# Kernel optimization log

Hardware: AMD Instinct MI355X
Metric: run time of the kernel (lower is better)

The kernel has to match this reference:

```python
import jax, jax.numpy as jnp
import numpy as np

B, S, V, E, H, A, L = 64, 256, 32000, 512, 512, 512, 2
EPS = 1e-5


def _ln(x, g, b):
    m = jnp.mean(x, axis=-1, keepdims=True)
    v = jnp.mean((x - m) ** 2, axis=-1, keepdims=True)
    return (x - m) * jax.lax.rsqrt(v + EPS) * g + b


def _lstm_cell(x, h, c, W_ih, W_hh, b_ih, b_hh):
    # torch gate order: i, f, g, o
    gates = x @ W_ih.T + b_ih + h @ W_hh.T + b_hh  # [B, 4H]
    i, f, g, o = jnp.split(gates, 4, axis=-1)
    i, f, o = jax.nn.sigmoid(i), jax.nn.sigmoid(f), jax.nn.sigmoid(o)
    g = jnp.tanh(g)
    c_new = f * c + i * g
    h_new = o * jnp.tanh(c_new)
    return h_new, c_new


def setup_inputs() -> dict:
    key = jax.random.key(0)
    ks = jax.random.split(key, 24)
    d = {}
    d['input_token'] = jax.random.randint(ks[0], (B, 1), 0, V)
    d['h0'] = jax.random.normal(ks[1], (L, B, H), jnp.float32)
    d['c0'] = jax.random.normal(ks[2], (L, B, H), jnp.float32)
    d['encoder_outputs'] = jax.random.normal(ks[3], (B, S, 2 * H), jnp.float32)
    d['encoder_mask'] = jnp.ones((B, S), jnp.int32)
    sc = lambda fi, fo: float(np.sqrt(6.0 / (fi + fo)))
    d['emb'] = jax.random.normal(ks[4], (V, E), jnp.float32) * 0.1
    d['ln_emb_g'] = jnp.ones((E,), jnp.float32)
    d['ln_emb_b'] = jnp.zeros((E,), jnp.float32)
    d['W_enc'] = jax.random.uniform(ks[5], (A, 2 * H), jnp.float32, -sc(2 * H, A), sc(2 * H, A))
    d['b_enc'] = jnp.zeros((A,), jnp.float32)
    d['W_dec'] = jax.random.uniform(ks[6], (A, H), jnp.float32, -sc(H, A), sc(H, A))
    d['b_dec'] = jnp.zeros((A,), jnp.float32)
    d['v_att'] = jax.random.uniform(ks[7], (1, A), jnp.float32, -sc(A, 1), sc(A, 1))
    d['ln_att_g'] = jnp.ones((A,), jnp.float32)
    d['ln_att_b'] = jnp.zeros((A,), jnp.float32)
    in0, in1 = E + 2 * H, H
    d['W_ih0'] = jax.random.uniform(ks[8], (4 * H, in0), jnp.float32, -sc(in0, 4 * H), sc(in0, 4 * H))
    d['W_hh0'] = jax.random.normal(ks[9], (4 * H, H), jnp.float32) * 0.05
    d['b_ih0'] = jnp.zeros((4 * H,), jnp.float32).at[H:2 * H].set(1.0)
    d['b_hh0'] = jnp.zeros((4 * H,), jnp.float32)
    d['W_ih1'] = jax.random.uniform(ks[10], (4 * H, in1), jnp.float32, -sc(in1, 4 * H), sc(in1, 4 * H))
    d['W_hh1'] = jax.random.normal(ks[11], (4 * H, H), jnp.float32) * 0.05
    d['b_ih1'] = jnp.zeros((4 * H,), jnp.float32).at[H:2 * H].set(1.0)
    d['b_hh1'] = jnp.zeros((4 * H,), jnp.float32)
    d['ln_lstm_g'] = jnp.ones((H,), jnp.float32)
    d['ln_lstm_b'] = jnp.zeros((H,), jnp.float32)
    d['W_ctx'] = jax.random.uniform(ks[12], (H, 2 * H), jnp.float32, -sc(2 * H, H), sc(2 * H, H))
    d['b_ctx'] = jnp.zeros((H,), jnp.float32)
    d['W_out'] = jax.random.uniform(ks[13], (V, H), jnp.float32, -sc(H, V), sc(H, V))
    d['b_out'] = jnp.zeros((V,), jnp.float32)
    return d


def reference(input_token, h0, c0, encoder_outputs, encoder_mask,
              emb, ln_emb_g, ln_emb_b,
              W_enc, b_enc, W_dec, b_dec, v_att, ln_att_g, ln_att_b,
              W_ih0, W_hh0, b_ih0, b_hh0, W_ih1, W_hh1, b_ih1, b_hh1,
              ln_lstm_g, ln_lstm_b, W_ctx, b_ctx, W_out, b_out):
    # embedding + norm (dropout = identity in eval)
    embedded = _ln(emb[input_token], ln_emb_g, ln_emb_b)  # [B,1,E]

    # attention using top-layer hidden state
    dec_h = h0[-1]  # [B,H]
    enc_proj = jnp.einsum('bsk,ak->bsa', encoder_outputs, W_enc) + b_enc
    dec_proj = dec_h @ W_dec.T + b_dec  # [B,A]
    combined = _ln(enc_proj + dec_proj[:, None, :], ln_att_g, ln_att_b)
    scores = jnp.einsum('bsa,a->bs', jnp.tanh(combined), v_att[0])
    scores = jnp.where(encoder_mask == 0, -jnp.inf, scores)
    attn_w = jax.nn.softmax(scores, axis=1)  # [B,S]
    context = jnp.einsum('bs,bsk->bk', attn_w, encoder_outputs)  # [B,2H]

    # single-step 2-layer LSTM
    x = jnp.concatenate([embedded[:, 0, :], context], axis=-1)  # [B,E+2H]
    h_l0, c_l0 = _lstm_cell(x, h0[0], c0[0], W_ih0, W_hh0, b_ih0, b_hh0)
    h_l1, c_l1 = _lstm_cell(h_l0, h0[1], c0[1], W_ih1, W_hh1, b_ih1, b_hh1)
    h_new = jnp.stack([h_l0, h_l1])
    c_new = jnp.stack([c_l0, c_l1])

    lstm_out = _ln(h_l1, ln_lstm_g, ln_lstm_b)  # [B,H]
    proj_ctx = context @ W_ctx.T + b_ctx  # [B,H]
    logits = (lstm_out + proj_ctx) @ W_out.T + b_out  # [B,V]
    return logits[:, None, :], (h_new, c_new), attn_w
```

## Files before the change

### kernel.cpp

```cpp
#include <hip/hip_runtime.h>

typedef unsigned int u32;
typedef unsigned short u16;
typedef __attribute__((ext_vector_type(8))) short short8;
typedef __attribute__((ext_vector_type(4))) float f32x4;

__device__ __forceinline__ float bf2f(u16 u) {
  union { u32 i; float f; } v; v.i = ((u32)u) << 16; return v.f;
}
__device__ __forceinline__ u16 f2bf(float f) {
  union { float f; u32 i; } v; v.f = f;
  u32 u = v.i;
  u += 0x7FFFu + ((u >> 16) & 1u);
  return (u16)(u >> 16);
}
__device__ __forceinline__ float tanh_fast(float x) {
  float e = __expf(-2.f * fabsf(x));
  float r = (1.f - e) / (1.f + e);
  return x < 0.f ? -r : r;
}
__device__ __forceinline__ float sigmoid_fast(float x) {
  return 1.f / (1.f + __expf(-x));
}
template<bool F32>
__device__ __forceinline__ float ld1(const void* p, size_t i) {
  return F32 ? ((const float*)p)[i] : bf2f(((const u16*)p)[i]);
}
__device__ __forceinline__ void outst(void* p, size_t i, float v, int f32o) {
  if (f32o) ((float*)p)[i] = v; else ((u16*)p)[i] = f2bf(v);
}

#define GLL16(gp, lp) __builtin_amdgcn_global_load_lds( \
    (__attribute__((address_space(1))) void*)(gp), \
    (__attribute__((address_space(3))) void*)(lp), 16, 0, 0)

#define OFF_H    2048000
#define OFF_C    2113536
#define OFF_ATTN 2179072

#define A_LNAG 0
#define A_LNAB 512
#define A_VAT  1024
#define A_BENC 1536
#define A_BDEC 2048
#define A_BIH0 2560
#define A_BHH0 4608
#define A_BIH1 6656
#define A_BHH1 8704
#define A_LNLG 10752
#define A_LNLB 11264
#define A_BCTX 11776
#define A_BOUT 12288
#define A_TOTAL 44288

struct SrcPtrs {
  const void *h0, *c0, *emb, *lneg, *lneb, *Wenc, *benc, *Wdec, *bdec, *vat,
             *lnag, *lnab, *bih0, *bhh0, *bih1, *bhh1, *lnlg, *lnlb, *Wctx,
             *bctx, *bout;
  const int *tok;
};

__global__ void k_flag(const u32* __restrict__ lneg, int* __restrict__ flag) {
  if (threadIdx.x == 0) flag[0] = (lneg[0] == 0x3F800000u) ? 1 : 0;
}

template<bool F32>
__device__ __forceinline__ void convblk(const void* src, u16* dst, size_t base) {
  size_t i0 = base + (size_t)threadIdx.x * 16;
  if (F32) {
    const float* s = (const float*)src + i0;
    float4 a = *(const float4*)s, b = *(const float4*)(s + 4);
    float4 c = *(const float4*)(s + 8), d = *(const float4*)(s + 12);
    short8 v0, v1;
    v0[0]=(short)f2bf(a.x); v0[1]=(short)f2bf(a.y); v0[2]=(short)f2bf(a.z); v0[3]=(short)f2bf(a.w);
    v0[4]=(short)f2bf(b.x); v0[5]=(short)f2bf(b.y); v0[6]=(short)f2bf(b.z); v0[7]=(short)f2bf(b.w);
    v1[0]=(short)f2bf(c.x); v1[1]=(short)f2bf(c.y); v1[2]=(short)f2bf(c.z); v1[3]=(short)f2bf(c.w);
    v1[4]=(short)f2bf(d.x); v1[5]=(short)f2bf(d.y); v1[6]=(short)f2bf(d.z); v1[7]=(short)f2bf(d.w);
    *(short8*)(dst + i0) = v0; *(short8*)(dst + i0 + 8) = v1;
  } else {
    const uint4* s = (const uint4*)((const u16*)src + i0);
    uint4 a = s[0], b = s[1];
    *(uint4*)(dst + i0) = a; *((uint4*)(dst + i0) + 1) = b;
  }
}

template<bool F32>
__global__ __launch_bounds__(256) void k_conv(
    const int* __restrict__ flagp, SrcPtrs P,
    u16* __restrict__ xcat, u16* __restrict__ xcat1, u16* __restrict__ h1bf,
    float* __restrict__ c0f, float* __restrict__ arena,
    u16* __restrict__ Wencbf, u16* __restrict__ Wdecbf, u16* __restrict__ Wctxbf)
{
  if (flagp[0] != (F32 ? 1 : 0)) return;
  __shared__ float red[8];
  const int t = threadIdx.x;
  const int blk = blockIdx.x;
  if (blk < 64) {
    const int b = blk;
    const int tk = P.tok[b];
    float e0 = ld1<F32>(P.emb, (size_t)tk * 512 + t);
    float e1 = ld1<F32>(P.emb, (size_t)tk * 512 + t + 256);
    float s = e0 + e1, ss = e0 * e0 + e1 * e1;
    #pragma unroll
    for (int o = 1; o < 64; o <<= 1) { s += __shfl_xor(s, o, 64); ss += __shfl_xor(ss, o, 64); }
    if ((t & 63) == 0) { red[t >> 6] = s; red[4 + (t >> 6)] = ss; }
    __syncthreads();
    s = red[0] + red[1] + red[2] + red[3];
    ss = red[4] + red[5] + red[6] + red[7];
    const float mean = s * (1.f / 512.f);
    const float rstd = rsqrtf(fmaxf(ss * (1.f / 512.f) - mean * mean, 0.f) + 1e-5f);
    xcat[b*2048 + t]       = f2bf((e0 - mean) * rstd * ld1<F32>(P.lneg, t) + ld1<F32>(P.lneb, t));
    xcat[b*2048 + t + 256] = f2bf((e1 - mean) * rstd * ld1<F32>(P.lneg, t + 256) + ld1<F32>(P.lneb, t + 256));
    xcat[b*2048 + 1536 + t]       = f2bf(ld1<F32>(P.h0, (size_t)b * 512 + t));
    xcat[b*2048 + 1536 + t + 256] = f2bf(ld1<F32>(P.h0, (size_t)b * 512 + t + 256));
  } else if (blk < 128) {
    const int b = blk - 64;
    for (int j = t; j < 512; j += 256) {
      float h1 = ld1<F32>(P.h0, 32768 + (size_t)b * 512 + j);
      xcat1[b*1024 + 512 + j] = f2bf(h1);
      h1bf[b*512 + j] = f2bf(h1);
      c0f[b*512 + j]         = ld1<F32>(P.c0, (size_t)b * 512 + j);
      c0f[32768 + b*512 + j] = ld1<F32>(P.c0, 32768 + (size_t)b * 512 + j);
    }
  } else if (blk < 256) {
    const int qb = (blk - 128) * 512;
    #pragma unroll
    for (int u = 0; u < 2; u++) {
      int Qi = qb + u * 256 + t;
      int kc = Qi >> 11, rem = Qi & 2047;
      int cq = rem >> 9, col = rem & 511;
      size_t src = (size_t)col * 1024 + kc * 32 + cq * 8;
      if (F32) {
        const float* s = (const float*)P.Wenc + src;
        float4 a = *(const float4*)s, b2 = *(const float4*)(s + 4);
        short8 v;
        v[0]=(short)f2bf(a.x); v[1]=(short)f2bf(a.y); v[2]=(short)f2bf(a.z); v[3]=(short)f2bf(a.w);
        v[4]=(short)f2bf(b2.x); v[5]=(short)f2bf(b2.y); v[6]=(short)f2bf(b2.z); v[7]=(short)f2bf(b2.w);
        *(short8*)(Wencbf + (size_t)Qi * 8) = v;
      } else {
        *(uint4*)(Wencbf + (size_t)Qi * 8) = *(const uint4*)((const u16*)P.Wenc + src);
      }
    }
  } else if (blk < 320) {
    convblk<F32>(P.Wdec, Wdecbf, (size_t)(blk - 256) * 4096);
  } else if (blk < 448) {
    convblk<F32>(P.Wctx, Wctxbf, (size_t)(blk - 320) * 4096);
  } else {
    int base = (blk - 448) * 4096;
    for (int i = t; i < 4096; i += 256) {
      int v = base + i;
      if (v >= A_TOTAL) break;
      const void* s; int off;
      if      (v < 512)   { s = P.lnag; off = v; }
      else if (v < 1024)  { s = P.lnab; off = v - 512; }
      else if (v < 1536)  { s = P.vat;  off = v - 1024; }
      else if (v < 2048)  { s = P.benc; off = v - 1536; }
      else if (v < 2560)  { s = P.bdec; off = v - 2048; }
      else if (v < 4608)  { s = P.bih0; off = v - 2560; }
      else if (v < 6656)  { s = P.bhh0; off = v - 4608; }
      else if (v < 8704)  { s = P.bih1; off = v - 6656; }
      else if (v < 10752) { s = P.bhh1; off = v - 8704; }
      else if (v < 11264) { s = P.lnlg; off = v - 10752; }
      else if (v < 11776) { s = P.lnlb; off = v - 11264; }
      else if (v < 12288) { s = P.bctx; off = v - 11776; }
      else                { s = P.bout; off = v - 12288; }
      arena[v] = ld1<F32>(s, off);
    }
  }
}

__global__ __launch_bounds__(256) void k_dproj(
    const u16* __restrict__ h1bf, const u16* __restrict__ Wdecbf,
    const float* __restrict__ arena, float* __restrict__ dpf)
{
  __shared__ float hs[512];
  __shared__ float part[256];
  const int t = threadIdx.x;
  const int b = blockIdx.x >> 2, cg = blockIdx.x & 3;
  {
    u32 u2 = *(const u32*)(h1bf + b * 512 + t * 2);
    hs[t * 2]     = bf2f((u16)(u2 & 0xffff));
    hs[t * 2 + 1] = bf2f((u16)(u2 >> 16));
  }
  __syncthreads();
  const int col = cg * 128 + (t & 127);
  const int kh = (t >> 7) * 256;
  const u16* w = Wdecbf + (size_t)col * 512 + kh;
  float acc = 0.f;
  #pragma unroll 4
  for (int k = 0; k < 256; k += 8) {
    short8 wv = *(const short8*)(w + k);
    #pragma unroll
    for (int i = 0; i < 8; i++) acc += hs[kh + k + i] * bf2f((u16)wv[i]);
  }
  part[t] = acc;
  __syncthreads();
  if (t < 128) {
    float v = part[t] + part[t + 128];
    dpf[b * 512 + col] = v + arena[A_BENC + col] + arena[A_BDEC + col];
  }
}

__global__ __launch_bounds__(512, 4) void k_scores(
    const int* __restrict__ flagp,
    const void* __restrict__ enc, const u16* __restrict__ WencT,
    const float* __restrict__ dpf, const float* __restrict__ arena,
    const int* __restrict__ mask, float* __restrict__ scores)
{
  const int f32w = flagp[0];
  __shared__ __align__(16) char sm[69632];
  const int t = threadIdx.x, wave = t >> 6, lane = t & 63;
  const int q = lane >> 4, r15 = lane & 15;
  const int m0 = blockIdx.x * 32, b = m0 >> 8, n0 = wave * 64;
  const int arow = t >> 2, acq = t & 3;

  float4 rA0, rA1;

  auto stageB = [&](int buf, int kt) {
    char* Bb = sm + buf * 32768;
    #pragma unroll
    for (int r = 0; r < 4; ++r) {
      int chunk = (wave << 2) + r;
      const u16* g = WencT + (size_t)kt * 16384 + (size_t)(chunk * 64 + lane) * 8;
      GLL16(g, Bb + chunk * 1024);
    }
  };
  auto stageAb = [&](int buf, int kc) {
    if (wave < 2) {
      int s = (wave << 6) + lane;
      int cq = s >> 5, rowslot = s & 31;
      int row = rowslot ^ (cq << 1);
      const u16* g = (const u16*)enc + (size_t)(m0 + row) * 1024 + kc + (cq << 3);
      GLL16(g, sm + 65536 + buf * 2048 + (wave << 10));
    }
  };
  auto issueAf = [&](int kc) {
    const float* p = (const float*)enc + (size_t)(m0 + arow) * 1024 + kc + (acq << 3);
    rA0 = *(const float4*)p; rA1 = *(const float4*)(p + 4);
  };
  auto writeAf = [&](int buf) {
    short8 v;
    v[0]=(short)f2bf(rA0.x); v[1]=(short)f2bf(rA0.y); v[2]=(short)f2bf(rA0.z); v[3]=(short)f2bf(rA0.w);
    v[4]=(short)f2bf(rA1.x); v[5]=(short)f2bf(rA1.y); v[6]=(short)f2bf(rA1.z); v[7]=(short)f2bf(rA1.w);
    int slot = (acq << 5) + (arow ^ (acq << 1));
    *(short8*)(sm + 65536 + buf * 2048 + slot * 16) = v;
  };

  if (f32w) { if (t < 128) issueAf(0); }
  stageB(0, 0);
  if (!f32w) stageAb(0, 0);
  if (f32w && t < 128) writeAf(0);
  __syncthreads();

  f32x4 acc[2][4] = {};
  int cur = 0;
  for (int kt = 0; kt < 32; ++kt) {
    const int more = (kt + 1 < 32);
    if (more) {
      if (f32w) { if (t < 128) issueAf((kt + 1) << 5); }
      stageB(cur ^ 1, kt + 1);
      if (!f32w) stageAb(cur ^ 1, (kt + 1) << 5);
    }
    const char* Ab = sm + 65536 + cur * 2048;
    const char* Bb = sm + cur * 32768;
    short8 af[2], bfr[4];
    #pragma unroll
    for (int mi = 0; mi < 2; mi++) {
      int slot = (q << 5) + ((mi * 16 + r15) ^ (q << 1));
      af[mi] = *(const short8*)(Ab + slot * 16);
    }
    #pragma unroll
    for (int ni = 0; ni < 4; ni++)
      bfr[ni] = *(const short8*)(Bb + ((q << 9) + n0 + ni * 16 + r15) * 16);
    #pragma unroll
    for (int mi = 0; mi < 2; mi++)
      #pragma unroll
      for (int ni = 0; ni < 4; ni++)
        acc[mi][ni] = __builtin_amdgcn_mfma_f32_16x16x32_bf16(af[mi], bfr[ni], acc[mi][ni], 0, 0, 0);
    if (more && f32w && t < 128) writeAf(cur ^ 1);
    __syncthreads();
    cur ^= 1;
  }

  float dpv[4];
  #pragma unroll
  for (int ni = 0; ni < 4; ni++)
    dpv[ni] = dpf[b * 512 + n0 + ni * 16 + r15];

  float* ps    = (float*)sm;
  float* pq    = (float*)(sm + 1024);
  float* mean_ = (float*)(sm + 2048);
  float* rstd_ = (float*)(sm + 2176);
  #pragma unroll
  for (int mi = 0; mi < 2; mi++)
    #pragma unroll
    for (int r = 0; r < 4; r++) {
      float s = 0.f, sq = 0.f;
      #pragma unroll
      for (int ni = 0; ni < 4; ni++) {
        float x = acc[mi][ni][r] + dpv[ni];
        s += x; sq += x * x;
      }
      #pragma unroll
      for (int o = 1; o < 16; o <<= 1) { s += __shfl_xor(s, o, 64); sq += __shfl_xor(sq, o, 64); }
      if (r15 == 0) { int row = mi*16 + q*4 + r; ps[wave*32 + row] = s; pq[wave*32 + row] = sq; }
    }
  __syncthreads();
  if (t < 32) {
    float s = 0.f, sq = 0.f;
    #pragma unroll
    for (int w = 0; w < 8; w++) { s += ps[w*32 + t]; sq += pq[w*32 + t]; }
    float mn = s * (1.f / 512.f);
    mean_[t] = mn;
    rstd_[t] = rsqrtf(fmaxf(sq * (1.f / 512.f) - mn * mn, 0.f) + 1e-5f);
  }
  __syncthreads();
  float g4[4], b4[4], v4[4];
  #pragma unroll
  for (int ni = 0; ni < 4; ni++) {
    int col = n0 + ni*16 + r15;
    g4[ni] = arena[A_LNAG + col]; b4[ni] = arena[A_LNAB + col]; v4[ni] = arena[A_VAT + col];
  }
  #pragma unroll
  for (int mi = 0; mi < 2; mi++)
    #pragma unroll
    for (int r = 0; r < 4; r++) {
      int row = mi*16 + q*4 + r;
      float mn = mean_[row], rs = rstd_[row];
      float s = 0.f;
      #pragma unroll
      for (int ni = 0; ni < 4; ni++) {
        float x = acc[mi][ni][r] + dpv[ni];
        float y = (x - mn) * rs * g4[ni] + b4[ni];
        s += tanh_fast(y) * v4[ni];
      }
      #pragma unroll
      for (int o = 1; o < 16; o <<= 1) s += __shfl_xor(s, o, 64);
      if (r15 == 0) ps[wave*32 + row] = s;
    }
  __syncthreads();
  if (t < 32) {
    float sc = 0.f;
    #pragma unroll
    for (int w = 0; w < 8; w++) sc += ps[w*32 + t];
    int s_ = (m0 & 255) + t;
    scores[m0 + t] = mask[b*256 + s_] ? sc : -__builtin_inff();
  }
}

__global__ __launch_bounds__(256) void k_softmax_ctx(
    const int* __restrict__ flagp,
    const float* __restrict__ scores, const void* __restrict__ enc,
    u16* __restrict__ xcat, void* __restrict__ out)
{
  const int f32w = flagp[0];
  __shared__ float aw[256];
  __shared__ float red[8];
  __shared__ float px[1024];
  const int t = threadIdx.x;
  const int b = blockIdx.x >> 2, kq = blockIdx.x & 3;
  float sv = scores[b * 256 + t];
  float mx = sv;
  #pragma unroll
  for (int o = 1; o < 64; o <<= 1) mx = fmaxf(mx, __shfl_xor(mx, o, 64));
  if ((t & 63) == 0) red[t >> 6] = mx;
  __syncthreads();
  mx = fmaxf(fmaxf(red[0], red[1]), fmaxf(red[2], red[3]));
  float e = __expf(sv - mx);
  float s = e;
  #pragma unroll
  for (int o = 1; o < 64; o <<= 1) s += __shfl_xor(s, o, 64);
  if ((t & 63) == 0) red[4 + (t >> 6)] = s;
  __syncthreads();
  s = red[4] + red[5] + red[6] + red[7];
  float w = e / s;
  aw[t] = w;
  if (kq == 0) outst(out, OFF_ATTN + b * 256 + t, w, f32w);
  __syncthreads();
  const int kk = t & 63, sg = t >> 6;
  float a0 = 0.f, a1 = 0.f, a2 = 0.f, a3 = 0.f;
  if (f32w) {
    const float* p = (const float*)enc + (size_t)b * 262144 + kq * 256 + kk * 4;
    #pragma unroll 8
    for (int i = 0; i < 64; i++) {
      int si = i * 4 + sg;
      float4 v = *(const float4*)(p + (size_t)si * 1024);
      float w_ = aw[si];
      a0 += w_ * v.x; a1 += w_ * v.y; a2 += w_ * v.z; a3 += w_ * v.w;
    }
  } else {
    const u16* p = (const u16*)enc + (size_t)b * 262144 + kq * 256 + kk * 4;
    #pragma unroll 8
    for (int i = 0; i < 64; i++) {
      int si = i * 4 + sg;
      uint2 u = *(const uint2*)(p + (size_t)si * 1024);
      float w_ = aw[si];
      a0 += w_ * bf2f((u16)(u.x & 0xffff)); a1 += w_ * bf2f((u16)(u.x >> 16));
      a2 += w_ * bf2f((u16)(u.y & 0xffff)); a3 += w_ * bf2f((u16)(u.y >> 16));
    }
  }
  px[sg * 256 + kk * 4]     = a0;
  px[sg * 256 + kk * 4 + 1] = a1;
  px[sg * 256 + kk * 4 + 2] = a2;
  px[sg * 256 + kk * 4 + 3] = a3;
  __syncthreads();
  float cv = px[t] + px[256 + t] + px[512 + t] + px[768 + t];
  xcat[b * 2048 + 512 + kq * 256 + t] = f2bf(cv);
}

__global__ __launch_bounds__(512) void k_lstm(
    const int* __restrict__ flagp,
    const u16* __restrict__ x, int K,
    const void* __restrict__ Wa, int Ka,
    const void* __restrict__ Wb, int Kb,
    int boff_ih, int boff_hh,
    const float* __restrict__ arena, const float* __restrict__ c0f, int coff,
    void* __restrict__ out, size_t h_off, size_t c_off,
    u16* __restrict__ aux_bf, float* __restrict__ aux_f)
{
  const int f32w = flagp[0];
  __shared__ __align__(16) char sm[40960];
  const int t = threadIdx.x, wave = t >> 6, lane = t & 63;
  const int q = lane >> 4, r15 = lane & 15;
  const int jt = blockIdx.x;
  const int kslice = K >> 3, ksteps = kslice >> 5;
  const int k0 = wave * kslice;
  const void* W; int Kw, koff;
  if (k0 < Ka) { W = Wa; Kw = Ka; koff = k0; }
  else         { W = Wb; Kw = Kb; koff = k0 - Ka; }
  char* slab = sm + wave * 5120;
  const int bc = lane >> 2, bcq = lane & 3;
  const int wrow = (bc >> 2) * 512 + jt * 4 + (bc & 3);
  f32x4 acc4[4] = {};

  for (int st = 0; st < ksteps; ++st) {
    const int kA = k0 + st * 32;
    const int kB = koff + st * 32;
    #pragma unroll
    for (int i = 0; i < 4; i++) {
      int id = i * 64 + lane;
      int row = id >> 2, cq = id & 3;
      *(uint4*)(slab + (cq * 64 + row) * 16) = *(const uint4*)(x + (size_t)row * K + kA + cq * 8);
    }
    {
      size_t wi = (size_t)wrow * Kw + kB + bcq * 8;
      short8 bv;
      if (f32w) {
        const float* wp = (const float*)W + wi;
        float4 a = *(const float4*)wp, b = *(const float4*)(wp + 4);
        bv[0]=(short)f2bf(a.x); bv[1]=(short)f2bf(a.y); bv[2]=(short)f2bf(a.z); bv[3]=(short)f2bf(a.w);
        bv[4]=(short)f2bf(b.x); bv[5]=(short)f2bf(b.y); bv[6]=(short)f2bf(b.z); bv[7]=(short)f2bf(b.w);
      } else {
        bv = *(const short8*)((const u16*)W + wi);
      }
      *(short8*)(slab + 4096 + (bcq * 16 + bc) * 16) = bv;
    }
    short8 af[4];
    #pragma unroll
    for (int mi = 0; mi < 4; mi++)
      af[mi] = *(const short8*)(slab + (q * 64 + mi * 16 + r15) * 16);
    short8 bfrg = *(const short8*)(slab + 4096 + (q * 16 + r15) * 16);
    #pragma unroll
    for (int mi = 0; mi < 4; mi++)
      acc4[mi] = __builtin_amdgcn_mfma_f32_16x16x32_bf16(af[mi], bfrg, acc4[mi], 0, 0, 0);
  }
  __syncthreads();
  float* part = (float*)sm;
  #pragma unroll
  for (int mi = 0; mi < 4; mi++)
    #pragma unroll
    for (int r = 0; r < 4; r++)
      part[wave * 1024 + (mi * 16 + q * 4 + r) * 16 + r15] = acc4[mi][r];
  __syncthreads();
  if (t < 256) {
    const int b_ = t >> 2, cl = t & 3;
    const int jg = jt * 4 + cl;
    float g4[4];
    #pragma unroll
    for (int g = 0; g < 4; g++) {
      float v = 0.f;
      #pragma unroll
      for (int w = 0; w < 8; w++) v += part[w * 1024 + b_ * 16 + g * 4 + cl];
      g4[g] = v + arena[boff_ih + g * 512 + jg] + arena[boff_hh + g * 512 + jg];
    }
    float i_ = sigmoid_fast(g4[0]), f_ = sigmoid_fast(g4[1]), o_ = sigmoid_fast(g4[3]);
    float gg = tanh_fast(g4[2]);
    float c_ = f_ * c0f[coff + b_ * 512 + jg] + i_ * gg;
    float h_ = o_ * tanh_fast(c_);
    outst(out, h_off + b_ * 512 + jg, h_, f32w);
    outst(out, c_off + b_ * 512 + jg, c_, f32w);
    if (aux_bf) aux_bf[b_ * 1024 + jg] = f2bf(h_);
    if (aux_f)  aux_f[b_ * 512 + jg] = h_;
  }
}

__global__ __launch_bounds__(256) void k_svec(
    const float* __restrict__ hl1f, const u16* __restrict__ xcat,
    const u16* __restrict__ Wctxbf, const float* __restrict__ arena,
    u16* __restrict__ svec)
{
  __shared__ float ctx[1024];
  __shared__ float red[8];
  const int t = threadIdx.x, b = blockIdx.x;
  for (int i = t; i < 1024; i += 256) ctx[i] = bf2f(xcat[b * 2048 + 512 + i]);
  float h0v = hl1f[b * 512 + t], h1v = hl1f[b * 512 + t + 256];
  float s = h0v + h1v, ss = h0v * h0v + h1v * h1v;
  #pragma unroll
  for (int o = 1; o < 64; o <<= 1) { s += __shfl_xor(s, o, 64); ss += __shfl_xor(ss, o, 64); }
  if ((t & 63) == 0) { red[t >> 6] = s; red[4 + (t >> 6)] = ss; }
  __syncthreads();
  s = red[0] + red[1] + red[2] + red[3];
  ss = red[4] + red[5] + red[6] + red[7];
  const float mean = s * (1.f / 512.f);
  const float rstd = rsqrtf(fmaxf(ss * (1.f / 512.f) - mean * mean, 0.f) + 1e-5f);
  for (int hh = t; hh < 512; hh += 256) {
    float hv = hl1f[b * 512 + hh];
    float lnv = (hv - mean) * rstd * arena[A_LNLG + hh] + arena[A_LNLB + hh];
    float acc = arena[A_BCTX + hh];
    #pragma unroll 4
    for (int k = 0; k < 1024; k += 8) {
      short8 wv = *(const short8*)(Wctxbf + (size_t)hh * 1024 + k);
      #pragma unroll
      for (int i = 0; i < 8; i++) acc += ctx[k + i] * bf2f((u16)wv[i]);
    }
    svec[b * 512 + hh] = f2bf(lnv + acc);
  }
}

__global__ __launch_bounds__(256) void k_logits(
    const int* __restrict__ flagp,
    const u16* __restrict__ svec, const void* __restrict__ Wout,
    const float* __restrict__ arena, void* __restrict__ out)
{
  const int f32w = flagp[0];
  __shared__ __align__(16) char sm[8192];
  const int t = threadIdx.x, wave = t >> 6, lane = t & 63;
  const int q = lane >> 4, r15 = lane & 15;
  const int nb = blockIdx.x * 64;
  const int row = t >> 2, cq = t & 3;
  float4 ra, rb; uint4 rc;
  auto issue = [&](int kc) {
    size_t off = (size_t)(nb + row) * 512 + kc * 32 + cq * 8;
    if (f32w) {
      const float* p = (const float*)Wout + off;
      ra = *(const float4*)p; rb = *(const float4*)(p + 4);
    } else {
      rc = *(const uint4*)((const u16*)Wout + off);
    }
  };
  auto wr = [&](int buf) {
    int slot = (cq << 6) + (row ^ (cq << 1));
    if (f32w) {
      short8 v;
      v[0]=(short)f2bf(ra.x); v[1]=(short)f2bf(ra.y); v[2]=(short)f2bf(ra.z); v[3]=(short)f2bf(ra.w);
      v[4]=(short)f2bf(rb.x); v[5]=(short)f2bf(rb.y); v[6]=(short)f2bf(rb.z); v[7]=(short)f2bf(rb.w);
      *(short8*)(sm + buf * 4096 + slot * 16) = v;
    } else {
      *(uint4*)(sm + buf * 4096 + slot * 16) = rc;
    }
  };
  issue(0);
  wr(0);
  __syncthreads();
  f32x4 acc[4] = {};
  int cur = 0;
  for (int kc = 0; kc < 16; kc++) {
    const int more = (kc + 1 < 16);
    if (more) issue(kc + 1);
    short8 af[4], bfr;
    #pragma unroll
    for (int mi = 0; mi < 4; mi++)
      af[mi] = *(const short8*)(svec + (size_t)(mi * 16 + r15) * 512 + kc * 32 + q * 8);
    {
      int col = wave * 16 + r15;
      int slot = (q << 6) + (col ^ (q << 1));
      bfr = *(const short8*)(sm + cur * 4096 + slot * 16);
    }
    #pragma unroll
    for (int mi = 0; mi < 4; mi++)
      acc[mi] = __builtin_amdgcn_mfma_f32_16x16x32_bf16(af[mi], bfr, acc[mi], 0, 0, 0);
    if (more) wr(cur ^ 1);
    __syncthreads();
    cur ^= 1;
  }
  {
    int col = nb + wave * 16 + r15;
    float bo = arena[A_BOUT + col];
    #pragma unroll
    for (int mi = 0; mi < 4; mi++)
      #pragma unroll
      for (int r = 0; r < 4; r++) {
        int brow = mi * 16 + q * 4 + r;
        outst(out, (size_t)brow * 32000 + col, acc[mi][r] + bo, f32w);
      }
  }
}

extern "C" void kernel_launch(void* const* d_in, const int* in_sizes, int n_in,
                              void* d_out, int out_size, void* d_ws, size_t ws_size,
                              hipStream_t stream)
{
  SrcPtrs P;
  P.tok  = (const int*)d_in[0];
  P.h0   = d_in[1];  P.c0   = d_in[2];
  const void* enc = d_in[3];
  const int* mask = (const int*)d_in[4];
  P.emb  = d_in[5]; P.lneg = d_in[6]; P.lneb = d_in[7];
  P.Wenc = d_in[8]; P.benc = d_in[9]; P.Wdec = d_in[10]; P.bdec = d_in[11];
  P.vat  = d_in[12]; P.lnag = d_in[13]; P.lnab = d_in[14];
  P.bih0 = d_in[17]; P.bhh0 = d_in[18];
  P.bih1 = d_in[21]; P.bhh1 = d_in[22];
  P.lnlg = d_in[23]; P.lnlb = d_in[24];
  P.Wctx = d_in[25]; P.bctx = d_in[26];
  const void* Wout = d_in[27];
  P.bout = d_in[28];
  const void* Wih0 = d_in[15];
  const void* Whh0 = d_in[16];
  const void* Wih1 = d_in[19];
  const void* Whh1 = d_in[20];

  char* ws = (char*)d_ws;
  int*   flag    = (int*)(ws + 0);
  float* arena   = (float*)(ws + 256);
  u16*   Wencbf  = (u16*)(ws + 177664);
  u16*   Wdecbf  = (u16*)(ws + 1226240);
  u16*   Wctxbf  = (u16*)(ws + 1750528);
  u16*   xcat    = (u16*)(ws + 2799104);
  u16*   xcat1   = (u16*)(ws + 3061248);
  u16*   h1bf    = (u16*)(ws + 3192320);
  float* c0f     = (float*)(ws + 3257856);
  float* scores  = (float*)(ws + 3520000);
  float* hl1f    = (float*)(ws + 3585536);
  u16*   svec    = (u16*)(ws + 3716608);
  float* dpf     = (float*)(ws + 3782144);

  k_flag<<<1, 64, 0, stream>>>((const u32*)P.lneg, flag);
  k_conv<false><<<460, 256, 0, stream>>>(flag, P, xcat, xcat1, h1bf, c0f, arena, Wencbf, Wdecbf, Wctxbf);
  k_conv<true ><<<460, 256, 0, stream>>>(flag, P, xcat, xcat1, h1bf, c0f, arena, Wencbf, Wdecbf, Wctxbf);
  k_dproj<<<256, 256, 0, stream>>>(h1bf, Wdecbf, arena, dpf);
  k_scores<<<512, 512, 0, stream>>>(flag, enc, Wencbf, dpf, arena, mask, scores);
  k_softmax_ctx<<<256, 256, 0, stream>>>(flag, scores, enc, xcat, d_out);
  k_lstm<<<128, 512, 0, stream>>>(flag, xcat, 2048, Wih0, 1536, Whh0, 512,
                                  A_BIH0, A_BHH0, arena, c0f, 0,
                                  d_out, OFF_H, OFF_C, xcat1, (float*)nullptr);
  k_lstm<<<128, 512, 0, stream>>>(flag, xcat1, 1024, Wih1, 512, Whh1, 512,
                                  A_BIH1, A_BHH1, arena, c0f, 32768,
                                  d_out, OFF_H + 32768, OFF_C + 32768,
                                  (u16*)nullptr, hl1f);
  k_svec<<<64, 256, 0, stream>>>(hl1f, xcat, Wctxbf, arena, svec);
  k_logits<<<500, 256, 0, stream>>>(flag, svec, Wout, arena, d_out);
}
```

Baseline: 390.8 us.

## Cut kernel launches, fuse decoder projection into conversion, and restage scores/logits loads

Result: faster. 358.8 us (-8.2%).

```diff
diff --git a/kernel.cpp b/kernel.cpp
--- a/kernel.cpp
+++ b/kernel.cpp
@@ -22,17 +22,15 @@
 __device__ __forceinline__ float sigmoid_fast(float x) {
   return 1.f / (1.f + __expf(-x));
 }
-template<bool F32>
-__device__ __forceinline__ float ld1(const void* p, size_t i) {
-  return F32 ? ((const float*)p)[i] : bf2f(((const u16*)p)[i]);
+__device__ __forceinline__ float ld1r(const void* p, size_t i, int f32w) {
+  return f32w ? ((const float*)p)[i] : bf2f(((const u16*)p)[i]);
 }
 __device__ __forceinline__ void outst(void* p, size_t i, float v, int f32o) {
   if (f32o) ((float*)p)[i] = v; else ((u16*)p)[i] = f2bf(v);
 }
-
-#define GLL16(gp, lp) __builtin_amdgcn_global_load_lds( \
-    (__attribute__((address_space(1))) void*)(gp), \
-    (__attribute__((address_space(3))) void*)(lp), 16, 0, 0)
+__device__ __forceinline__ int flag_of(const u32* lnegp) {
+  return (lnegp[0] == 0x3F800000u) ? 1 : 0;
+}
 
 #define OFF_H    2048000
 #define OFF_C    2113536
@@ -60,14 +58,9 @@
   const int *tok;
 };
 
-__global__ void k_flag(const u32* __restrict__ lneg, int* __restrict__ flag) {
-  if (threadIdx.x == 0) flag[0] = (lneg[0] == 0x3F800000u) ? 1 : 0;
-}
-
-template<bool F32>
-__device__ __forceinline__ void convblk(const void* src, u16* dst, size_t base) {
+__device__ __forceinline__ void convblk_r(const void* src, u16* dst, size_t base, int f32w) {
   size_t i0 = base + (size_t)threadIdx.x * 16;
-  if (F32) {
+  if (f32w) {
     const float* s = (const float*)src + i0;
     float4 a = *(const float4*)s, b = *(const float4*)(s + 4);
     float4 c = *(const float4*)(s + 8), d = *(const float4*)(s + 12);
@@ -84,22 +77,24 @@
   }
 }
 
-template<bool F32>
 __global__ __launch_bounds__(256) void k_conv(
-    const int* __restrict__ flagp, SrcPtrs P,
-    u16* __restrict__ xcat, u16* __restrict__ xcat1, u16* __restrict__ h1bf,
+    const u32* __restrict__ lnegp, SrcPtrs P,
+    u16* __restrict__ xcat, u16* __restrict__ xcat1,
     float* __restrict__ c0f, float* __restrict__ arena,
-    u16* __restrict__ Wencbf, u16* __restrict__ Wdecbf, u16* __restrict__ Wctxbf)
+    u16* __restrict__ Wencbf, u16* __restrict__ Wctxbf,
+    float* __restrict__ dpf)
 {
-  if (flagp[0] != (F32 ? 1 : 0)) return;
+  const int f32w = flag_of(lnegp);
   __shared__ float red[8];
+  __shared__ float hs[512];
+  __shared__ float part[256];
   const int t = threadIdx.x;
   const int blk = blockIdx.x;
   if (blk < 64) {
     const int b = blk;
     const int tk = P.tok[b];
-    float e0 = ld1<F32>(P.emb, (size_t)tk * 512 + t);
-    float e1 = ld1<F32>(P.emb, (size_t)tk * 512 + t + 256);
+    float e0 = ld1r(P.emb, (size_t)tk * 512 + t, f32w);
+    float e1 = ld1r(P.emb, (size_t)tk * 512 + t + 256, f32w);
     float s = e0 + e1, ss = e0 * e0 + e1 * e1;
     #pragma unroll
     for (int o = 1; o < 64; o <<= 1) { s += __shfl_xor(s, o, 64); ss += __shfl_xor(ss, o, 64); }
@@ -109,18 +104,17 @@
     ss = red[4] + red[5] + red[6] + red[7];
     const float mean = s * (1.f / 512.f);
     const float rstd = rsqrtf(fmaxf(ss * (1.f / 512.f) - mean * mean, 0.f) + 1e-5f);
-    xcat[b*2048 + t]       = f2bf((e0 - mean) * rstd * ld1<F32>(P.lneg, t) + ld1<F32>(P.lneb, t));
-    xcat[b*2048 + t + 256] = f2bf((e1 - mean) * rstd * ld1<F32>(P.lneg, t + 256) + ld1<F32>(P.lneb, t + 256));
-    xcat[b*2048 + 1536 + t]       = f2bf(ld1<F32>(P.h0, (size_t)b * 512 + t));
-    xcat[b*2048 + 1536 + t + 256] = f2bf(ld1<F32>(P.h0, (size_t)b * 512 + t + 256));
+    xcat[b*2048 + t]       = f2bf((e0 - mean) * rstd * ld1r(P.lneg, t, f32w) + ld1r(P.lneb, t, f32w));
+    xcat[b*2048 + t + 256] = f2bf((e1 - mean) * rstd * ld1r(P.lneg, t + 256, f32w) + ld1r(P.lneb, t + 256, f32w));
+    xcat[b*2048 + 1536 + t]       = f2bf(ld1r(P.h0, (size_t)b * 512 + t, f32w));
+    xcat[b*2048 + 1536 + t + 256] = f2bf(ld1r(P.h0, (size_t)b * 512 + t + 256, f32w));
   } else if (blk < 128) {
     const int b = blk - 64;
     for (int j = t; j < 512; j += 256) {
-      float h1 = ld1<F32>(P.h0, 32768 + (size_t)b * 512 + j);
+      float h1 = ld1r(P.h0, 32768 + (size_t)b * 512 + j, f32w);
       xcat1[b*1024 + 512 + j] = f2bf(h1);
-      h1bf[b*512 + j] = f2bf(h1);
-      c0f[b*512 + j]         = ld1<F32>(P.c0, (size_t)b * 512 + j);
-      c0f[32768 + b*512 + j] = ld1<F32>(P.c0, 32768 + (size_t)b * 512 + j);
+      c0f[b*512 + j]         = ld1r(P.c0, (size_t)b * 512 + j, f32w);
+      c0f[32768 + b*512 + j] = ld1r(P.c0, 32768 + (size_t)b * 512 + j, f32w);
     }
   } else if (blk < 256) {
     const int qb = (blk - 128) * 512;
@@ -130,7 +124,7 @@
       int kc = Qi >> 11, rem = Qi & 2047;
       int cq = rem >> 9, col = rem & 511;
       size_t src = (size_t)col * 1024 + kc * 32 + cq * 8;
-      if (F32) {
+      if (f32w) {
         const float* s = (const float*)P.Wenc + src;
         float4 a = *(const float4*)s, b2 = *(const float4*)(s + 4);
         short8 v;
@@ -141,12 +135,47 @@
         *(uint4*)(Wencbf + (size_t)Qi * 8) = *(const uint4*)((const u16*)P.Wenc + src);
       }
     }
-  } else if (blk < 320) {
-    convblk<F32>(P.Wdec, Wdecbf, (size_t)(blk - 256) * 4096);
-  } else if (blk < 448) {
-    convblk<F32>(P.Wctx, Wctxbf, (size_t)(blk - 320) * 4096);
+  } else if (blk < 384) {
+    convblk_r(P.Wctx, Wctxbf, (size_t)(blk - 256) * 4096, f32w);
+  } else if (blk < 640) {
+    const int db = blk - 384;
+    const int b2 = db >> 2, cg = db & 3;
+    if (f32w) {
+      float2 v = *(const float2*)((const float*)P.h0 + 32768 + (size_t)b2 * 512 + t * 2);
+      hs[t * 2] = v.x; hs[t * 2 + 1] = v.y;
+    } else {
+      u32 u2 = *(const u32*)((const u16*)P.h0 + 32768 + (size_t)b2 * 512 + t * 2);
+      hs[t * 2] = bf2f((u16)(u2 & 0xffff)); hs[t * 2 + 1] = bf2f((u16)(u2 >> 16));
+    }
+    __syncthreads();
+    const int col = cg * 128 + (t & 127);
+    const int kh = (t >> 7) * 256;
+    float acc = 0.f;
+    if (f32w) {
+      const float* wp = (const float*)P.Wdec + (size_t)col * 512 + kh;
+      #pragma unroll 4
+      for (int k = 0; k < 256; k += 8) {
+        float4 a = *(const float4*)(wp + k), b4 = *(const float4*)(wp + k + 4);
+        acc += hs[kh+k]*a.x + hs[kh+k+1]*a.y + hs[kh+k+2]*a.z + hs[kh+k+3]*a.w
+             + hs[kh+k+4]*b4.x + hs[kh+k+5]*b4.y + hs[kh+k+6]*b4.z + hs[kh+k+7]*b4.w;
+      }
+    } else {
+      const u16* wp = (const u16*)P.Wdec + (size_t)col * 512 + kh;
+      #pragma unroll 4
+      for (int k = 0; k < 256; k += 8) {
+        short8 wv = *(const short8*)(wp + k);
+        #pragma unroll
+        for (int i = 0; i < 8; i++) acc += hs[kh + k + i] * bf2f((u16)wv[i]);
+      }
+    }
+    part[t] = acc;
+    __syncthreads();
+    if (t < 128) {
+      float v = part[t] + part[t + 128];
+      dpf[b2 * 512 + col] = v + ld1r(P.benc, col, f32w) + ld1r(P.bdec, col, f32w);
+    }
   } else {
-    int base = (blk - 448) * 4096;
+    int base = (blk - 640) * 4096;
     for (int i = t; i < 4096; i += 256) {
       int v = base + i;
       if (v >= A_TOTAL) break;
@@ -164,122 +193,91 @@
       else if (v < 11776) { s = P.lnlb; off = v - 11264; }
       else if (v < 12288) { s = P.bctx; off = v - 11776; }
       else                { s = P.bout; off = v - 12288; }
-      arena[v] = ld1<F32>(s, off);
-    }
-  }
-}
-
-__global__ __launch_bounds__(256) void k_dproj(
-    const u16* __restrict__ h1bf, const u16* __restrict__ Wdecbf,
-    const float* __restrict__ arena, float* __restrict__ dpf)
-{
-  __shared__ float hs[512];
-  __shared__ float part[256];
-  const int t = threadIdx.x;
-  const int b = blockIdx.x >> 2, cg = blockIdx.x & 3;
-  {
-    u32 u2 = *(const u32*)(h1bf + b * 512 + t * 2);
-    hs[t * 2]     = bf2f((u16)(u2 & 0xffff));
-    hs[t * 2 + 1] = bf2f((u16)(u2 >> 16));
-  }
-  __syncthreads();
-  const int col = cg * 128 + (t & 127);
-  const int kh = (t >> 7) * 256;
-  const u16* w = Wdecbf + (size_t)col * 512 + kh;
-  float acc = 0.f;
-  #pragma unroll 4
-  for (int k = 0; k < 256; k += 8) {
-    short8 wv = *(const short8*)(w + k);
-    #pragma unroll
-    for (int i = 0; i < 8; i++) acc += hs[kh + k + i] * bf2f((u16)wv[i]);
-  }
-  part[t] = acc;
-  __syncthreads();
-  if (t < 128) {
-    float v = part[t] + part[t + 128];
-    dpf[b * 512 + col] = v + arena[A_BENC + col] + arena[A_BDEC + col];
+      arena[v] = ld1r(s, off, f32w);
+    }
   }
 }
 
 __global__ __launch_bounds__(512, 4) void k_scores(
-    const int* __restrict__ flagp,
+    const u32* __restrict__ lnegp,
     const void* __restrict__ enc, const u16* __restrict__ WencT,
     const float* __restrict__ dpf, const float* __restrict__ arena,
     const int* __restrict__ mask, float* __restrict__ scores)
 {
-  const int f32w = flagp[0];
-  __shared__ __align__(16) char sm[69632];
+  const int f32w = flag_of(lnegp);
+  __shared__ __align__(16) char sm[8192];
   const int t = threadIdx.x, wave = t >> 6, lane = t & 63;
   const int q = lane >> 4, r15 = lane & 15;
   const int m0 = blockIdx.x * 32, b = m0 >> 8, n0 = wave * 64;
   const int arow = t >> 2, acq = t & 3;
-
-  float4 rA0, rA1;
-
-  auto stageB = [&](int buf, int kt) {
-    char* Bb = sm + buf * 32768;
-    #pragma unroll
-    for (int r = 0; r < 4; ++r) {
-      int chunk = (wave << 2) + r;
-      const u16* g = WencT + (size_t)kt * 16384 + (size_t)(chunk * 64 + lane) * 8;
-      GLL16(g, Bb + chunk * 1024);
-    }
+  const int aslot = ((acq << 5) + (arow ^ (acq << 1))) * 16;
+
+  const u16* bp = WencT + (size_t)((q << 9) + n0 + r15) * 8;
+  const float* aF = (const float*)enc + (size_t)(m0 + arow) * 1024 + (acq << 3);
+  const u16*   aH = (const u16*)enc   + (size_t)(m0 + arow) * 1024 + (acq << 3);
+
+  short8 Bst[2][4];
+  float4 Af[2][2];
+  uint4  Au[2];
+
+  auto issueB = [&](int set, int kt) {
+    const u16* p = bp + (size_t)kt * 16384;
+    Bst[set][0] = *(const short8*)(p);
+    Bst[set][1] = *(const short8*)(p + 128);
+    Bst[set][2] = *(const short8*)(p + 256);
+    Bst[set][3] = *(const short8*)(p + 384);
   };
-  auto stageAb = [&](int buf, int kc) {
-    if (wave < 2) {
-      int s = (wave << 6) + lane;
-      int cq = s >> 5, rowslot = s & 31;
-      int row = rowslot ^ (cq << 1);
-      const u16* g = (const u16*)enc + (size_t)(m0 + row) * 1024 + kc + (cq << 3);
-      GLL16(g, sm + 65536 + buf * 2048 + (wave << 10));
+  auto issueA = [&](int set, int kc) {
+    if (f32w) {
+      const float* p = aF + kc;
+      Af[set][0] = *(const float4*)p;
+      Af[set][1] = *(const float4*)(p + 4);
+    } else {
+      Au[set] = *(const uint4*)(aH + kc);
     }
   };
-  auto issueAf = [&](int kc) {
-    const float* p = (const float*)enc + (size_t)(m0 + arow) * 1024 + kc + (acq << 3);
-    rA0 = *(const float4*)p; rA1 = *(const float4*)(p + 4);
+  auto writeA = [&](int buf, int set) {
+    short8 v;
+    if (f32w) {
+      float4 a = Af[set][0], b2 = Af[set][1];
+      v[0]=(short)f2bf(a.x); v[1]=(short)f2bf(a.y); v[2]=(short)f2bf(a.z); v[3]=(short)f2bf(a.w);
+      v[4]=(short)f2bf(b2.x); v[5]=(short)f2bf(b2.y); v[6]=(short)f2bf(b2.z); v[7]=(short)f2bf(b2.w);
+    } else {
+      union { uint4 u; short8 s; } cv; cv.u = Au[set]; v = cv.s;
+    }
+    *(short8*)(sm + buf * 2048 + aslot) = v;
   };
-  auto writeAf = [&](int buf) {
-    short8 v;
-    v[0]=(short)f2bf(rA0.x); v[1]=(short)f2bf(rA0.y); v[2]=(short)f2bf(rA0.z); v[3]=(short)f2bf(rA0.w);
-    v[4]=(short)f2bf(rA1.x); v[5]=(short)f2bf(rA1.y); v[6]=(short)f2bf(rA1.z); v[7]=(short)f2bf(rA1.w);
-    int slot = (acq << 5) + (arow ^ (acq << 1));
-    *(short8*)(sm + 65536 + buf * 2048 + slot * 16) = v;
-  };
-
-  if (f32w) { if (t < 128) issueAf(0); }
-  stageB(0, 0);
-  if (!f32w) stageAb(0, 0);
-  if (f32w && t < 128) writeAf(0);
-  __syncthreads();
+
+  if (t < 128) { issueA(1, 0); issueA(0, 32); }
+  issueB(0, 0);
+  if (t < 128) writeA(0, 1);
+  __builtin_amdgcn_sched_barrier(0);
+  asm volatile("s_waitcnt lgkmcnt(0)" ::: "memory");
+  __builtin_amdgcn_s_barrier();
+  __builtin_amdgcn_sched_barrier(0);
 
   f32x4 acc[2][4] = {};
-  int cur = 0;
+  #pragma unroll 2
   for (int kt = 0; kt < 32; ++kt) {
-    const int more = (kt + 1 < 32);
-    if (more) {
-      if (f32w) { if (t < 128) issueAf((kt + 1) << 5); }
-      stageB(cur ^ 1, kt + 1);
-      if (!f32w) stageAb(cur ^ 1, (kt + 1) << 5);
-    }
-    const char* Ab = sm + 65536 + cur * 2048;
-    const char* Bb = sm + cur * 32768;
-    short8 af[2], bfr[4];
+    const int cur = kt & 1, nxt = cur ^ 1;
+    if (t < 128) issueA(nxt, ((kt + 2 < 32) ? (kt + 2) : 31) << 5);
+    issueB(nxt, (kt + 1 < 32) ? (kt + 1) : 31);
+    short8 af[2];
     #pragma unroll
     for (int mi = 0; mi < 2; mi++) {
       int slot = (q << 5) + ((mi * 16 + r15) ^ (q << 1));
-      af[mi] = *(const short8*)(Ab + slot * 16);
-    }
-    #pragma unroll
-    for (int ni = 0; ni < 4; ni++)
-      bfr[ni] = *(const short8*)(Bb + ((q << 9) + n0 + ni * 16 + r15) * 16);
+      af[mi] = *(const short8*)(sm + cur * 2048 + slot * 16);
+    }
     #pragma unroll
     for (int mi = 0; mi < 2; mi++)
       #pragma unroll
       for (int ni = 0; ni < 4; ni++)
-        acc[mi][ni] = __builtin_amdgcn_mfma_f32_16x16x32_bf16(af[mi], bfr[ni], acc[mi][ni], 0, 0, 0);
-    if (more && f32w && t < 128) writeAf(cur ^ 1);
-    __syncthreads();
-    cur ^= 1;
+        acc[mi][ni] = __builtin_amdgcn_mfma_f32_16x16x32_bf16(af[mi], Bst[cur][ni], acc[mi][ni], 0, 0, 0);
+    if (t < 128 && kt + 1 < 32) writeA(nxt, cur);
+    __builtin_amdgcn_sched_barrier(0);
+    asm volatile("s_waitcnt lgkmcnt(0)" ::: "memory");
+    __builtin_amdgcn_s_barrier();
+    __builtin_amdgcn_sched_barrier(0);
   }
 
   float dpv[4];
@@ -287,10 +285,10 @@
   for (int ni = 0; ni < 4; ni++)
     dpv[ni] = dpf[b * 512 + n0 + ni * 16 + r15];
 
-  float* ps    = (float*)sm;
-  float* pq    = (float*)(sm + 1024);
-  float* mean_ = (float*)(sm + 2048);
-  float* rstd_ = (float*)(sm + 2176);
+  float* ps    = (float*)(sm + 4096);
+  float* pq    = (float*)(sm + 5120);
+  float* mean_ = (float*)(sm + 6144);
+  float* rstd_ = (float*)(sm + 6272);
   #pragma unroll
   for (int mi = 0; mi < 2; mi++)
     #pragma unroll
@@ -349,11 +347,11 @@
 }
 
 __global__ __launch_bounds__(256) void k_softmax_ctx(
-    const int* __restrict__ flagp,
+    const u32* __restrict__ lnegp,
     const float* __restrict__ scores, const void* __restrict__ enc,
     u16* __restrict__ xcat, void* __restrict__ out)
 {
-  const int f32w = flagp[0];
+  const int f32w = flag_of(lnegp);
   __shared__ float aw[256];
   __shared__ float red[8];
   __shared__ float px[1024];
@@ -409,7 +407,7 @@
 }
 
 __global__ __launch_bounds__(512) void k_lstm(
-    const int* __restrict__ flagp,
+    const u32* __restrict__ lnegp,
     const u16* __restrict__ x, int K,
     const void* __restrict__ Wa, int Ka,
     const void* __restrict__ Wb, int Kb,
@@ -418,29 +416,30 @@
     void* __restrict__ out, size_t h_off, size_t c_off,
     u16* __restrict__ aux_bf, float* __restrict__ aux_f)
 {
-  const int f32w = flagp[0];
-  __shared__ __align__(16) char sm[40960];
+  const int f32w = flag_of(lnegp);
+  __shared__ __align__(16) char sm[24576];
   const int t = threadIdx.x, wave = t >> 6, lane = t & 63;
   const int q = lane >> 4, r15 = lane & 15;
-  const int jt = blockIdx.x;
+  const int jt = blockIdx.x & 127, bh = blockIdx.x >> 7;
   const int kslice = K >> 3, ksteps = kslice >> 5;
   const int k0 = wave * kslice;
   const void* W; int Kw, koff;
   if (k0 < Ka) { W = Wa; Kw = Ka; koff = k0; }
   else         { W = Wb; Kw = Kb; koff = k0 - Ka; }
-  char* slab = sm + wave * 5120;
+  char* slab = sm + wave * 3072;
   const int bc = lane >> 2, bcq = lane & 3;
   const int wrow = (bc >> 2) * 512 + jt * 4 + (bc & 3);
-  f32x4 acc4[4] = {};
+  f32x4 acc4[2] = {};
 
   for (int st = 0; st < ksteps; ++st) {
     const int kA = k0 + st * 32;
     const int kB = koff + st * 32;
     #pragma unroll
-    for (int i = 0; i < 4; i++) {
+    for (int i = 0; i < 2; i++) {
       int id = i * 64 + lane;
       int row = id >> 2, cq = id & 3;
-      *(uint4*)(slab + (cq * 64 + row) * 16) = *(const uint4*)(x + (size_t)row * K + kA + cq * 8);
+      *(uint4*)(slab + (cq * 32 + row) * 16) =
+          *(const uint4*)(x + (size_t)(bh * 32 + row) * K + kA + cq * 8);
     }
     {
       size_t wi = (size_t)wrow * Kw + kB + bcq * 8;
@@ -453,44 +452,45 @@
       } else {
         bv = *(const short8*)((const u16*)W + wi);
       }
-      *(short8*)(slab + 4096 + (bcq * 16 + bc) * 16) = bv;
-    }
-    short8 af[4];
-    #pragma unroll
-    for (int mi = 0; mi < 4; mi++)
-      af[mi] = *(const short8*)(slab + (q * 64 + mi * 16 + r15) * 16);
-    short8 bfrg = *(const short8*)(slab + 4096 + (q * 16 + r15) * 16);
-    #pragma unroll
-    for (int mi = 0; mi < 4; mi++)
+      *(short8*)(slab + 2048 + (bcq * 16 + bc) * 16) = bv;
+    }
+    short8 af[2];
+    #pragma unroll
+    for (int mi = 0; mi < 2; mi++)
+      af[mi] = *(const short8*)(slab + (q * 32 + mi * 16 + r15) * 16);
+    short8 bfrg = *(const short8*)(slab + 2048 + (q * 16 + r15) * 16);
+    #pragma unroll
+    for (int mi = 0; mi < 2; mi++)
       acc4[mi] = __builtin_amdgcn_mfma_f32_16x16x32_bf16(af[mi], bfrg, acc4[mi], 0, 0, 0);
   }
   __syncthreads();
   float* part = (float*)sm;
   #pragma unroll
-  for (int mi = 0; mi < 4; mi++)
+  for (int mi = 0; mi < 2; mi++)
     #pragma unroll
     for (int r = 0; r < 4; r++)
-      part[wave * 1024 + (mi * 16 + q * 4 + r) * 16 + r15] = acc4[mi][r];
-  __syncthreads();
-  if (t < 256) {
+      part[wave * 512 + (mi * 16 + q * 4 + r) * 16 + r15] = acc4[mi][r];
+  __syncthreads();
+  if (t < 128) {
     const int b_ = t >> 2, cl = t & 3;
+    const int bg = bh * 32 + b_;
     const int jg = jt * 4 + cl;
     float g4[4];
     #pragma unroll
     for (int g = 0; g < 4; g++) {
       float v = 0.f;
       #pragma unroll
-      for (int w = 0; w < 8; w++) v += part[w * 1024 + b_ * 16 + g * 4 + cl];
+      for (int w = 0; w < 8; w++) v += part[w * 512 + b_ * 16 + g * 4 + cl];
       g4[g] = v + arena[boff_ih + g * 512 + jg] + arena[boff_hh + g * 512 + jg];
     }
     float i_ = sigmoid_fast(g4[0]), f_ = sigmoid_fast(g4[1]), o_ = sigmoid_fast(g4[3]);
     float gg = tanh_fast(g4[2]);
-    float c_ = f_ * c0f[coff + b_ * 512 + jg] + i_ * gg;
+    float c_ = f_ * c0f[coff + bg * 512 + jg] + i_ * gg;
     float h_ = o_ * tanh_fast(c_);
-    outst(out, h_off + b_ * 512 + jg, h_, f32w);
-    outst(out, c_off + b_ * 512 + jg, c_, f32w);
-    if (aux_bf) aux_bf[b_ * 1024 + jg] = f2bf(h_);
-    if (aux_f)  aux_f[b_ * 512 + jg] = h_;
+    outst(out, h_off + bg * 512 + jg, h_, f32w);
+    outst(out, c_off + bg * 512 + jg, c_, f32w);
+    if (aux_bf) aux_bf[bg * 1024 + jg] = f2bf(h_);
+    if (aux_f)  aux_f[bg * 512 + jg] = h_;
   }
 }
 
@@ -501,7 +501,7 @@
 {
   __shared__ float ctx[1024];
   __shared__ float red[8];
-  const int t = threadIdx.x, b = blockIdx.x;
+  const int t = threadIdx.x, b = blockIdx.x >> 1, hf = blockIdx.x & 1;
   for (int i = t; i < 1024; i += 256) ctx[i] = bf2f(xcat[b * 2048 + 512 + i]);
   float h0v = hl1f[b * 512 + t], h1v = hl1f[b * 512 + t + 256];
   float s = h0v + h1v, ss = h0v * h0v + h1v * h1v;
@@ -513,87 +513,57 @@
   ss = red[4] + red[5] + red[6] + red[7];
   const float mean = s * (1.f / 512.f);
   const float rstd = rsqrtf(fmaxf(ss * (1.f / 512.f) - mean * mean, 0.f) + 1e-5f);
-  for (int hh = t; hh < 512; hh += 256) {
-    float hv = hl1f[b * 512 + hh];
-    float lnv = (hv - mean) * rstd * arena[A_LNLG + hh] + arena[A_LNLB + hh];
-    float acc = arena[A_BCTX + hh];
-    #pragma unroll 4
-    for (int k = 0; k < 1024; k += 8) {
-      short8 wv = *(const short8*)(Wctxbf + (size_t)hh * 1024 + k);
-      #pragma unroll
-      for (int i = 0; i < 8; i++) acc += ctx[k + i] * bf2f((u16)wv[i]);
-    }
-    svec[b * 512 + hh] = f2bf(lnv + acc);
-  }
+  const int hh = hf * 256 + t;
+  float hv = hl1f[b * 512 + hh];
+  float lnv = (hv - mean) * rstd * arena[A_LNLG + hh] + arena[A_LNLB + hh];
+  float acc = arena[A_BCTX + hh];
+  #pragma unroll 4
+  for (int k = 0; k < 1024; k += 8) {
+    short8 wv = *(const short8*)(Wctxbf + (size_t)hh * 1024 + k);
+    #pragma unroll
+    for (int i = 0; i < 8; i++) acc += ctx[k + i] * bf2f((u16)wv[i]);
+  }
+  svec[b * 512 + hh] = f2bf(lnv + acc);
 }
 
 __global__ __launch_bounds__(256) void k_logits(
-    const int* __restrict__ flagp,
+    const u32* __restrict__ lnegp,
     const u16* __restrict__ svec, const void* __restrict__ Wout,
     const float* __restrict__ arena, void* __restrict__ out)
 {
-  const int f32w = flagp[0];
-  __shared__ __align__(16) char sm[8192];
+  const int f32w = flag_of(lnegp);
   const int t = threadIdx.x, wave = t >> 6, lane = t & 63;
   const int q = lane >> 4, r15 = lane & 15;
-  const int nb = blockIdx.x * 64;
-  const int row = t >> 2, cq = t & 3;
-  float4 ra, rb; uint4 rc;
-  auto issue = [&](int kc) {
-    size_t off = (size_t)(nb + row) * 512 + kc * 32 + cq * 8;
+  const int col = blockIdx.x * 64 + wave * 16 + r15;
+  const float* wF = (const float*)Wout + (size_t)col * 512 + (q << 3);
+  const u16*   wH = (const u16*)Wout   + (size_t)col * 512 + (q << 3);
+  const u16*   sv = svec + (size_t)r15 * 512 + (q << 3);
+  f32x4 acc[4] = {};
+  #pragma unroll 4
+  for (int kc = 0; kc < 16; ++kc) {
+    short8 bfr;
     if (f32w) {
-      const float* p = (const float*)Wout + off;
-      ra = *(const float4*)p; rb = *(const float4*)(p + 4);
+      float4 a = *(const float4*)(wF + (kc << 5));
+      float4 b2 = *(const float4*)(wF + (kc << 5) + 4);
+      bfr[0]=(short)f2bf(a.x); bfr[1]=(short)f2bf(a.y); bfr[2]=(short)f2bf(a.z); bfr[3]=(short)f2bf(a.w);
+      bfr[4]=(short)f2bf(b2.x); bfr[5]=(short)f2bf(b2.y); bfr[6]=(short)f2bf(b2.z); bfr[7]=(short)f2bf(b2.w);
     } else {
-      rc = *(const uint4*)((const u16*)Wout + off);
-    }
-  };
-  auto wr = [&](int buf) {
-    int slot = (cq << 6) + (row ^ (cq << 1));
-    if (f32w) {
-      short8 v;
-      v[0]=(short)f2bf(ra.x); v[1]=(short)f2bf(ra.y); v[2]=(short)f2bf(ra.z); v[3]=(short)f2bf(ra.w);
-      v[4]=(short)f2bf(rb.x); v[5]=(short)f2bf(rb.y); v[6]=(short)f2bf(rb.z); v[7]=(short)f2bf(rb.w);
-      *(short8*)(sm + buf * 4096 + slot * 16) = v;
-    } else {
-      *(uint4*)(sm + buf * 4096 + slot * 16) = rc;
-    }
-  };
-  issue(0);
-  wr(0);
-  __syncthreads();
-  f32x4 acc[4] = {};
-  int cur = 0;
-  for (int kc = 0; kc < 16; kc++) {
-    const int more = (kc + 1 < 16);
-    if (more) issue(kc + 1);
-    short8 af[4], bfr;
-    #pragma unroll
-    for (int mi = 0; mi < 4; mi++)
-      af[mi] = *(const short8*)(svec + (size_t)(mi * 16 + r15) * 512 + kc * 32 + q * 8);
-    {
-      int col = wave * 16 + r15;
-      int slot = (q << 6) + (col ^ (q << 1));
-      bfr = *(const short8*)(sm + cur * 4096 + slot * 16);
-    }
-    #pragma unroll
-    for (int mi = 0; mi < 4; mi++)
-      acc[mi] = __builtin_amdgcn_mfma_f32_16x16x32_bf16(af[mi], bfr, acc[mi], 0, 0, 0);
-    if (more) wr(cur ^ 1);
-    __syncthreads();
-    cur ^= 1;
-  }
-  {
-    int col = nb + wave * 16 + r15;
-    float bo = arena[A_BOUT + col];
-    #pragma unroll
-    for (int mi = 0; mi < 4; mi++)
-      #pragma unroll
-      for (int r = 0; r < 4; r++) {
-        int brow = mi * 16 + q * 4 + r;
-        outst(out, (size_t)brow * 32000 + col, acc[mi][r] + bo, f32w);
-      }
-  }
+      bfr = *(const short8*)(wH + (kc << 5));
+    }
+    #pragma unroll
+    for (int mi = 0; mi < 4; mi++) {
+      short8 af = *(const short8*)(sv + (size_t)(mi * 16) * 512 + (kc << 5));
+      acc[mi] = __builtin_amdgcn_mfma_f32_16x16x32_bf16(af, bfr, acc[mi], 0, 0, 0);
+    }
+  }
+  float bo = arena[A_BOUT + col];
+  #pragma unroll
+  for (int mi = 0; mi < 4; mi++)
+    #pragma unroll
+    for (int r = 0; r < 4; r++) {
+      int brow = mi * 16 + q * 4 + r;
+      outst(out, (size_t)brow * 32000 + col, acc[mi][r] + bo, f32w);
+    }
 }
 
 extern "C" void kernel_launch(void* const* d_in, const int* in_sizes, int n_in,
@@ -618,35 +588,30 @@
   const void* Whh0 = d_in[16];
   const void* Wih1 = d_in[19];
   const void* Whh1 = d_in[20];
+  const u32* lnegp = (const u32*)P.lneg;
 
   char* ws = (char*)d_ws;
-  int*   flag    = (int*)(ws + 0);
   float* arena   = (float*)(ws + 256);
   u16*   Wencbf  = (u16*)(ws + 177664);
-  u16*   Wdecbf  = (u16*)(ws + 1226240);
   u16*   Wctxbf  = (u16*)(ws + 1750528);
   u16*   xcat    = (u16*)(ws + 2799104);
   u16*   xcat1   = (u16*)(ws + 3061248);
-  u16*   h1bf    = (u16*)(ws + 3192320);
   float* c0f     = (float*)(ws + 3257856);
   float* scores  = (float*)(ws + 3520000);
   float* hl1f    = (float*)(ws + 3585536);
   u16*   svec    = (u16*)(ws + 3716608);
   float* dpf     = (float*)(ws + 3782144);
 
-  k_flag<<<1, 64, 0, stream>>>((const u32*)P.lneg, flag);
-  k_conv<false><<<460, 256, 0, stream>>>(flag, P, xcat, xcat1, h1bf, c0f, arena, Wencbf, Wdecbf, Wctxbf);
-  k_conv<true ><<<460, 256, 0, stream>>>(flag, P, xcat, xcat1, h1bf, c0f, arena, Wencbf, Wdecbf, Wctxbf);
-  k_dproj<<<256, 256, 0, stream>>>(h1bf, Wdecbf, arena, dpf);
-  k_scores<<<512, 512, 0, stream>>>(flag, enc, Wencbf, dpf, arena, mask, scores);
-  k_softmax_ctx<<<256, 256, 0, stream>>>(flag, scores, enc, xcat, d_out);
-  k_lstm<<<128, 512, 0, stream>>>(flag, xcat, 2048, Wih0, 1536, Whh0, 512,
+  k_conv<<<651, 256, 0, stream>>>(lnegp, P, xcat, xcat1, c0f, arena, Wencbf, Wctxbf, dpf);
+  k_scores<<<512, 512, 0, stream>>>(lnegp, enc, Wencbf, dpf, arena, mask, scores);
+  k_softmax_ctx<<<256, 256, 0, stream>>>(lnegp, scores, enc, xcat, d_out);
+  k_lstm<<<256, 512, 0, stream>>>(lnegp, xcat, 2048, Wih0, 1536, Whh0, 512,
                                   A_BIH0, A_BHH0, arena, c0f, 0,
                                   d_out, OFF_H, OFF_C, xcat1, (float*)nullptr);
-  k_lstm<<<128, 512, 0, stream>>>(flag, xcat1, 1024, Wih1, 512, Whh1, 512,
+  k_lstm<<<256, 512, 0, stream>>>(lnegp, xcat1, 1024, Wih1, 512, Whh1, 512,
                                   A_BIH1, A_BHH1, arena, c0f, 32768,
                                   d_out, OFF_H + 32768, OFF_C + 32768,
                                   (u16*)nullptr, hl1f);
-  k_svec<<<64, 256, 0, stream>>>(hl1f, xcat, Wctxbf, arena, svec);
-  k_logits<<<500, 256, 0, stream>>>(flag, svec, Wout, arena, d_out);
-}
+  k_svec<<<128, 256, 0, stream>>>(hl1f, xcat, Wctxbf, arena, svec);
+  k_logits<<<500, 256, 0, stream>>>(lnegp, svec, Wout, arena, d_out);
+}
```
